# Performance work log

Hardware: AMD Instinct MI355X
Metric: run time of the kernel (lower is better)

The kernel has to match this reference:

```python
import jax, jax.numpy as jnp
import numpy as np

N = 100000   # total nodes in batch
E = 200000   # total edges
G = 4000     # number of graphs
H = 128      # gin_size = gin_hidden = gin_mlp_hidden = linear_hidden
L = 2        # gin_layers


def setup_inputs() -> dict:
    key = jax.random.key(0)
    ks = jax.random.split(key, 24)
    rn = lambda i, shape, s=0.05: (jax.random.normal(ks[i], shape, jnp.float32) * s)
    inp = dict(
        x=rn(0, (N, 14), 1.0),
        edge_attr=rn(1, (E, 4), 1.0),
        edge_index=jax.random.randint(ks[2], (2, E), 0, N, dtype=jnp.int32),
        batch=jnp.sort(jax.random.randint(ks[3], (N,), 0, G, dtype=jnp.int32)),
        node_w=rn(4, (14, H)), node_b=jnp.zeros((H,), jnp.float32),
        edge_w=rn(5, (4, H)), edge_b=jnp.zeros((H,), jnp.float32),
        eps=jnp.zeros((L,), jnp.float32),
        gin_w1=rn(6, (L, H, H)), gin_b1=jnp.zeros((L, H), jnp.float32),
        gin_w2=rn(7, (L, H, H)), gin_b2=jnp.zeros((L, H), jnp.float32),
        em_w1=rn(8, (L, H, H)), em_b1=jnp.zeros((L, H), jnp.float32),
        em_w2=rn(9, (L, H, H)), em_b2=jnp.zeros((L, H), jnp.float32),
        gru_wih=rn(10, (3 * H, H)), gru_whh=rn(11, (3 * H, H)),
        gru_bih=jnp.zeros((3 * H,), jnp.float32), gru_bhh=jnp.zeros((3 * H,), jnp.float32),
        lstm_wih=rn(12, (4 * H, 2 * H)), lstm_whh=rn(13, (4 * H, H)),
        lstm_bih=jnp.zeros((4 * H,), jnp.float32), lstm_bhh=jnp.zeros((4 * H,), jnp.float32),
        fc_w1=rn(14, (2 * H, H)), fc_b1=jnp.zeros((H,), jnp.float32),
        fc_w2=rn(15, (H, 1)), fc_b2=jnp.zeros((1,), jnp.float32),
    )
    return inp


def reference(x, edge_attr, edge_index, batch,
              node_w, node_b, edge_w, edge_b, eps,
              gin_w1, gin_b1, gin_w2, gin_b2,
              em_w1, em_b1, em_w2, em_b2,
              gru_wih, gru_whh, gru_bih, gru_bhh,
              lstm_wih, lstm_whh, lstm_bih, lstm_bhh,
              fc_w1, fc_b1, fc_w2, fc_b2):
    src, dst = edge_index[0], edge_index[1]
    node = x @ node_w + node_b          # [N,H]
    edge = edge_attr @ edge_w + edge_b  # [E,H]
    h = node                            # GRU hidden state
    for l in range(L):
        # GINEConv: msg = relu(x_src + e), scatter-add to dst, (1+eps)*x + agg, then MLP
        msg = jax.nn.relu(node[src] + edge)                     # [E,H] gather
        agg = jax.ops.segment_sum(msg, dst, num_segments=N)     # [N,H] scatter-add
        z = (1.0 + eps[l]) * node + agg
        m = jax.nn.relu(z @ gin_w1[l] + gin_b1[l]) @ gin_w2[l] + gin_b2[l]
        # GRU cell (seq_len=1)
        gi = m @ gru_wih.T + gru_bih
        gh = h @ gru_whh.T + gru_bhh
        ir, iz, inn = jnp.split(gi, 3, axis=-1)
        hr, hz, hn = jnp.split(gh, 3, axis=-1)
        r = jax.nn.sigmoid(ir + hr)
        zt = jax.nn.sigmoid(iz + hz)
        n = jnp.tanh(inn + r * hn)
        h = (1.0 - zt) * n + zt * h
        node = h
        # edge feature update MLP
        edge = jax.nn.relu(edge @ em_w1[l] + em_b1[l]) @ em_w2[l] + em_b2[l]
    # Set2Set pooling, processing_steps=3
    qs = jnp.zeros((G, 2 * H), node.dtype)
    hl = jnp.zeros((G, H), node.dtype)
    cl = jnp.zeros((G, H), node.dtype)
    for _ in range(3):
        g = qs @ lstm_wih.T + lstm_bih + hl @ lstm_whh.T + lstm_bhh
        i_, f_, g_, o_ = jnp.split(g, 4, axis=-1)
        cl = jax.nn.sigmoid(f_) * cl + jax.nn.sigmoid(i_) * jnp.tanh(g_)
        hl = jax.nn.sigmoid(o_) * jnp.tanh(cl)
        q = hl                                                   # [G,H]
        e = jnp.sum(node * q[batch], axis=-1)                    # [N]
        emax = jax.ops.segment_max(e, batch, num_segments=G)
        ex = jnp.exp(e - emax[batch])
        denom = jax.ops.segment_sum(ex, batch, num_segments=G)
        a = ex / jnp.maximum(denom, 1e-9)[batch]                 # per-graph softmax
        r = jax.ops.segment_sum(a[:, None] * node, batch, num_segments=G)  # [G,H]
        qs = jnp.concatenate([q, r], axis=-1)                    # [G,2H]
    out = jax.nn.relu(qs @ fc_w1 + fc_b1) @ fc_w2 + fc_b2
    return out.reshape(-1)
```

## Files before the change

kernel.cpp:

```cpp
#include <hip/hip_runtime.h>
#include <hip/hip_bf16.h>

constexpr int TN = 100000;
constexpr int TE = 200000;
constexpr int TG = 4000;
constexpr int TH = 128;

using short8 = __attribute__((ext_vector_type(8))) short;
using f32x4  = __attribute__((ext_vector_type(4))) float;
typedef __hip_bfloat16 bf16;

#define DEVINL __device__ __forceinline__
DEVINL float sigm(float x)  { return 1.f / (1.f + __expf(-x)); }
DEVINL float ftanh(float x) { return 1.f - 2.f / (__expf(2.f * x) + 1.f); }
DEVINL void unpack8(uint4 v, float* f) {
    const ushort* u = (const ushort*)&v;
#pragma unroll
    for (int j = 0; j < 8; ++j) f[j] = __bfloat162float(*(const bf16*)&u[j]);
}

__global__ void convAll(const float* __restrict__ g1, const float* __restrict__ g2,
                        const float* __restrict__ e1, const float* __restrict__ e2,
                        const float* __restrict__ gwih, const float* __restrict__ gwhh,
                        const float* __restrict__ lwih, const float* __restrict__ lwhh,
                        bf16* __restrict__ w6, bf16* __restrict__ wgru,
                        bf16* __restrict__ wl) {
    int i = blockIdx.x * 256 + threadIdx.x;
    if (i < 6 * TH * TH) {
        int m = i >> 14, r = i & 16383;
        int n = r >> 7, k = r & 127;
        const float* s = (m == 0) ? g1 : (m == 1) ? g1 + TH * TH
                       : (m == 2) ? g2 : (m == 3) ? g2 + TH * TH
                       : (m == 4) ? e1 : e2;
        w6[i] = __float2bfloat16(s[k * TH + n]);
        return;
    }
    i -= 6 * TH * TH;
    if (i < 2 * 384 * TH) {
        const float* s = (i < 384 * TH) ? gwih : gwhh;
        int r = (i < 384 * TH) ? i : i - 384 * TH;
        wgru[i] = __float2bfloat16(s[r]);
        return;
    }
    i -= 2 * 384 * TH;
    if (i < 512 * 256) {
        int c = i >> 8, k = i & 255;
        float v = (k < 128) ? lwih[c * 256 + k] + lwhh[c * 128 + k] : lwih[c * 256 + k];
        wl[i] = __float2bfloat16(v);
    }
}

template<int K>
__global__ __launch_bounds__(256) void proj64(const float* __restrict__ X,
                                              const float* __restrict__ W,
                                              const float* __restrict__ b,
                                              ushort* __restrict__ out, int M) {
    __shared__ float xs[64][K];
    int tid = threadIdx.x;
    int bm = blockIdx.x * 64;
    for (int i = tid; i < 64 * K; i += 256) {
        int r = i / K, k = i % K;
        xs[r][k] = (bm + r < M) ? X[(size_t)(bm + r) * K + k] : 0.f;
    }
    __syncthreads();
    int rb = tid >> 4, h0 = (tid & 15) * 8;
    float acc[4][8];
#pragma unroll
    for (int j = 0; j < 4; ++j)
#pragma unroll
        for (int c = 0; c < 8; ++c) acc[j][c] = b[h0 + c];
#pragma unroll
    for (int k = 0; k < K; ++k) {
        float4 w0 = *(const float4*)(W + k * TH + h0);
        float4 w1 = *(const float4*)(W + k * TH + h0 + 4);
#pragma unroll
        for (int j = 0; j < 4; ++j) {
            float xv = xs[rb + 16 * j][k];
            acc[j][0] = fmaf(xv, w0.x, acc[j][0]); acc[j][1] = fmaf(xv, w0.y, acc[j][1]);
            acc[j][2] = fmaf(xv, w0.z, acc[j][2]); acc[j][3] = fmaf(xv, w0.w, acc[j][3]);
            acc[j][4] = fmaf(xv, w1.x, acc[j][4]); acc[j][5] = fmaf(xv, w1.y, acc[j][5]);
            acc[j][6] = fmaf(xv, w1.z, acc[j][6]); acc[j][7] = fmaf(xv, w1.w, acc[j][7]);
        }
    }
#pragma unroll
    for (int j = 0; j < 4; ++j) {
        int row = bm + rb + 16 * j;
        if (row >= M) continue;
        ushort o[8];
#pragma unroll
        for (int c = 0; c < 8; ++c) {
            bf16 v = __float2bfloat16(acc[j][c]);
            o[c] = *(ushort*)&v;
        }
        *(uint4*)(out + (size_t)row * TH + h0) = *(uint4*)o;
    }
}

__global__ __launch_bounds__(256) void proj_scatter(
    const float* __restrict__ X, const float* __restrict__ W,
    const float* __restrict__ b, const int* __restrict__ perm,
    ushort* __restrict__ out, int M) {
    __shared__ float xs[64][4];
    int tid = threadIdx.x;
    int bm = blockIdx.x * 64;
    if (tid < 64) {
        float4 a = make_float4(0.f, 0.f, 0.f, 0.f);
        if (bm + tid < M) a = *(const float4*)(X + (size_t)(bm + tid) * 4);
        xs[tid][0] = a.x; xs[tid][1] = a.y; xs[tid][2] = a.z; xs[tid][3] = a.w;
    }
    __syncthreads();
    int rb = tid >> 4, h0 = (tid & 15) * 8;
    float acc[4][8];
#pragma unroll
    for (int j = 0; j < 4; ++j)
#pragma unroll
        for (int c = 0; c < 8; ++c) acc[j][c] = b[h0 + c];
#pragma unroll
    for (int k = 0; k < 4; ++k) {
        float4 w0 = *(const float4*)(W + k * TH + h0);
        float4 w1 = *(const float4*)(W + k * TH + h0 + 4);
#pragma unroll
        for (int j = 0; j < 4; ++j) {
            float xv = xs[rb + 16 * j][k];
            acc[j][0] = fmaf(xv, w0.x, acc[j][0]); acc[j][1] = fmaf(xv, w0.y, acc[j][1]);
            acc[j][2] = fmaf(xv, w0.z, acc[j][2]); acc[j][3] = fmaf(xv, w0.w, acc[j][3]);
            acc[j][4] = fmaf(xv, w1.x, acc[j][4]); acc[j][5] = fmaf(xv, w1.y, acc[j][5]);
            acc[j][6] = fmaf(xv, w1.z, acc[j][6]); acc[j][7] = fmaf(xv, w1.w, acc[j][7]);
        }
    }
#pragma unroll
    for (int j = 0; j < 4; ++j) {
        int row = bm + rb + 16 * j;
        if (row >= M) continue;
        ushort o[8];
#pragma unroll
        for (int c = 0; c < 8; ++c) {
            bf16 v = __float2bfloat16(acc[j][c]);
            o[c] = *(ushort*)&v;
        }
        *(uint4*)(out + (size_t)perm[row] * TH + h0) = *(uint4*)o;
    }
}

__global__ void count_deg(const int* __restrict__ ei_dst, int* __restrict__ deg, int En) {
    int e = blockIdx.x * 256 + threadIdx.x;
    if (e < En) atomicAdd(&deg[ei_dst[e]], 1);
}
__global__ void scan_block(const int* __restrict__ deg, int* __restrict__ rowptr,
                           int* __restrict__ bsum, int Nn) {
    __shared__ int sm[256];
    int tid = threadIdx.x;
    int gid = blockIdx.x * 256 + tid;
    int v = (gid < Nn) ? deg[gid] : 0;
    int x = v;
    sm[tid] = x; __syncthreads();
    for (int off = 1; off < 256; off <<= 1) {
        int t = (tid >= off) ? sm[tid - off] : 0;
        __syncthreads();
        x += t; sm[tid] = x;
        __syncthreads();
    }
    if (gid < Nn) rowptr[gid] = x - v;
    if (tid == 255) bsum[blockIdx.x] = x;
}
__global__ void scan_bsum(const int* __restrict__ bsum, int* __restrict__ bsumx, int nb) {
    __shared__ int sm[512];
    int tid = threadIdx.x;
    int v = (tid < nb) ? bsum[tid] : 0;
    int x = v;
    sm[tid] = x; __syncthreads();
    for (int off = 1; off < 512; off <<= 1) {
        int t = (tid >= off) ? sm[tid - off] : 0;
        __syncthreads();
        x += t; sm[tid] = x;
        __syncthreads();
    }
    if (tid < nb) bsumx[tid] = x - v;
}
__global__ void add_off(int* __restrict__ rowptr, const int* __restrict__ bsumx,
                        int Nn, int Etot) {
    int gid = blockIdx.x * 256 + threadIdx.x;
    if (gid < Nn) rowptr[gid] += bsumx[gid >> 8];
    if (gid == 0) rowptr[Nn] = Etot;
}
__global__ void fill_csr(const int* __restrict__ ei_src, const int* __restrict__ ei_dst,
                         const int* __restrict__ rowptr, int* __restrict__ cur,
                         int* __restrict__ srcp, int* __restrict__ epos, int En) {
    int e = blockIdx.x * 256 + threadIdx.x;
    if (e >= En) return;
    int d = ei_dst[e];
    int p = atomicAdd(&cur[d], 1);
    int slot = rowptr[d] + p;
    srcp[slot] = ei_src[e];
    epos[e] = slot;
}
__global__ void build_gptr(const int* __restrict__ batch, int* __restrict__ gptr,
                           int Nn, int Gn) {
    int n = blockIdx.x * 256 + threadIdx.x;
    if (n >= Nn) return;
    int bc = batch[n];
    int bp = (n == 0) ? -1 : batch[n - 1];
    for (int g = bp + 1; g <= bc; ++g) gptr[g] = n;
    if (n == Nn - 1) for (int g = bc + 1; g <= Gn; ++g) gptr[g] = Nn;
}

__global__ __launch_bounds__(256) void aggregate_v8(
    const ushort* __restrict__ node, const ushort* __restrict__ ef,
    const int* __restrict__ srcp, const int* __restrict__ rowptr,
    const float* __restrict__ eps, int l, ushort* __restrict__ zb, int Nn) {
    int t = blockIdx.x * 256 + threadIdx.x;
    int n = t >> 4;
    if (n >= Nn) return;
    int c8 = (t & 15) * 8;
    float se = 1.f + eps[l];
    float acc[8];
    uint4 nv = *(const uint4*)(node + (size_t)n * TH + c8);
    unpack8(nv, acc);
#pragma unroll
    for (int j = 0; j < 8; ++j) acc[j] *= se;
    int s0 = rowptr[n], s1 = rowptr[n + 1];
    int i = s0;
    for (; i + 1 < s1; i += 2) {
        int sa = srcp[i], sb = srcp[i + 1];
        uint4 av0 = *(const uint4*)(node + (size_t)sa * TH + c8);
        uint4 bv0 = *(const uint4*)(ef + (size_t)i * TH + c8);
        uint4 av1 = *(const uint4*)(node + (size_t)sb * TH + c8);
        uint4 bv1 = *(const uint4*)(ef + (size_t)(i + 1) * TH + c8);
        float a0[8], b0[8], a1[8], b1[8];
        unpack8(av0, a0); unpack8(bv0, b0);
        unpack8(av1, a1); unpack8(bv1, b1);
#pragma unroll
        for (int j = 0; j < 8; ++j)
            acc[j] += fmaxf(a0[j] + b0[j], 0.f) + fmaxf(a1[j] + b1[j], 0.f);
    }
    if (i < s1) {
        int sa = srcp[i];
        uint4 av = *(const uint4*)(node + (size_t)sa * TH + c8);
        uint4 bv = *(const uint4*)(ef + (size_t)i * TH + c8);
        float af[8], bf[8];
        unpack8(av, af); unpack8(bv, bf);
#pragma unroll
        for (int j = 0; j < 8; ++j) acc[j] += fmaxf(af[j] + bf[j], 0.f);
    }
    ushort o[8];
#pragma unroll
    for (int j = 0; j < 8; ++j) {
        bf16 v = __float2bfloat16(acc[j]);
        o[j] = *(ushort*)&v;
    }
    *(uint4*)(zb + (size_t)n * TH + c8) = *(uint4*)o;
}

__global__ __launch_bounds__(256) void mlp2_fused(
    const ushort* __restrict__ A, const ushort* __restrict__ W1t,
    const float* __restrict__ b1, const ushort* __restrict__ W2t,
    const float* __restrict__ b2, ushort* __restrict__ C, int M)
{
    __shared__ ushort As[128 * 128];
    __shared__ ushort Ts[128 * 128];
    const int tid = threadIdx.x;
    const int bm = blockIdx.x * 128;
    const int lane = tid & 63, w = tid >> 6;
    const int lr = lane & 15, lq = lane >> 4;
    const int wm = (w & 1) * 64, wn = (w >> 1) * 64;
    short8 wf[4][4];
#pragma unroll
    for (int ni = 0; ni < 4; ++ni)
#pragma unroll
        for (int ks = 0; ks < 4; ++ks)
            wf[ni][ks] = *(const short8*)(W1t + (size_t)(wn + ni * 16 + lr) * 128 + ks * 32 + lq * 8);
#pragma unroll
    for (int p = 0; p < 8; ++p) {
        int ch = p * 256 + tid;
        int r = ch >> 4, c = ch & 15;
        int row = bm + r;
        uint4 v = make_uint4(0u, 0u, 0u, 0u);
        if (row < M) v = *(const uint4*)(A + (size_t)row * 128 + c * 8);
        *(uint4*)(&As[r * 128 + ((c ^ (r & 15)) * 8)]) = v;
    }
    __syncthreads();
    {
        f32x4 acc[4][4] = {};
#pragma unroll
        for (int ks = 0; ks < 4; ++ks) {
            int cb = ks * 4 + lq;
            short8 af[4];
#pragma unroll
            for (int mi = 0; mi < 4; ++mi)
                af[mi] = *(const short8*)(&As[(wm + mi * 16 + lr) * 128 + ((cb ^ lr) * 8)]);
#pragma unroll
            for (int mi = 0; mi < 4; ++mi)
#pragma unroll
                for (int ni = 0; ni < 4; ++ni)
                    acc[mi][ni] = __builtin_amdgcn_mfma_f32_16x16x32_bf16(af[mi], wf[ni][ks], acc[mi][ni], 0, 0, 0);
        }
#pragma unroll
        for (int mi = 0; mi < 4; ++mi)
#pragma unroll
            for (int reg = 0; reg < 4; ++reg) {
                int row = wm + mi * 16 + lq * 4 + reg;
#pragma unroll
                for (int ni = 0; ni < 4; ++ni) {
                    int col = wn + ni * 16 + lr;
                    float v = fmaxf(acc[mi][ni][reg] + b1[col], 0.f);
                    bf16 bv = __float2bfloat16(v);
                    Ts[row * 128 + (((col >> 3) ^ (row & 15)) * 8) + (col & 7)] = *(ushort*)&bv;
                }
            }
    }
#pragma unroll
    for (int ni = 0; ni < 4; ++ni)
#pragma unroll
        for (int ks = 0; ks < 4; ++ks)
            wf[ni][ks] = *(const short8*)(W2t + (size_t)(wn + ni * 16 + lr) * 128 + ks * 32 + lq * 8);
    __syncthreads();
    {
        f32x4 acc[4][4] = {};
#pragma unroll
        for (int ks = 0; ks < 4; ++ks) {
            int cb = ks * 4 + lq;
            short8 af[4];
#pragma unroll
            for (int mi = 0; mi < 4; ++mi)
                af[mi] = *(const short8*)(&Ts[(wm + mi * 16 + lr) * 128 + ((cb ^ lr) * 8)]);
#pragma unroll
            for (int mi = 0; mi < 4; ++mi)
#pragma unroll
                for (int ni = 0; ni < 4; ++ni)
                    acc[mi][ni] = __builtin_amdgcn_mfma_f32_16x16x32_bf16(af[mi], wf[ni][ks], acc[mi][ni], 0, 0, 0);
        }
#pragma unroll
        for (int mi = 0; mi < 4; ++mi)
#pragma unroll
            for (int reg = 0; reg < 4; ++reg) {
                int row = bm + wm + mi * 16 + lq * 4 + reg;
                if (row >= M) continue;
#pragma unroll
                for (int ni = 0; ni < 4; ++ni) {
                    int col = wn + ni * 16 + lr;
                    bf16 bv = __float2bfloat16(acc[mi][ni][reg] + b2[col]);
                    C[(size_t)row * 128 + col] = *(ushort*)&bv;
                }
            }
    }
}

__global__ __launch_bounds__(512, 4) void gru_fused(
    const ushort* __restrict__ mfeat, const ushort* __restrict__ wih,
    const ushort* __restrict__ whh, const float* __restrict__ bih,
    const float* __restrict__ bhh, ushort* __restrict__ node, int Nn)
{
    __shared__ ushort Ms[64 * 128];
    __shared__ ushort Hs[64 * 128];
    const int tid = threadIdx.x;
    const int bm = blockIdx.x * 64;
#pragma unroll
    for (int p = 0; p < 4; ++p) {
        int ch = p * 512 + tid;
        bool isH = ch >= 1024;
        int r = (ch >> 4) & 63, c = ch & 15;
        int row = bm + r;
        uint4 v = make_uint4(0u, 0u, 0u, 0u);
        if (row < Nn) v = *(const uint4*)((isH ? node : mfeat) + (size_t)row * 128 + c * 8);
        ushort* dst = isH ? Hs : Ms;
        *(uint4*)(&dst[r * 128 + ((c ^ (r & 15)) * 8)]) = v;
    }
    __syncthreads();
    const int lane = tid & 63, w = tid >> 6;
    const int lr = lane & 15, lq = lane >> 4;
    const int col = w * 16 + lr;
    f32x4 aR[4] = {}, aZ[4] = {}, aN[4] = {}, aH[4] = {};
#pragma unroll
    for (int ks = 0; ks < 4; ++ks) {
        int koff = ks * 32 + lq * 8;
        short8 wv0 = *(const short8*)(wih + (size_t)col * 128 + koff);
        short8 wv1 = *(const short8*)(wih + (size_t)(128 + col) * 128 + koff);
        short8 wv2 = *(const short8*)(wih + (size_t)(256 + col) * 128 + koff);
        short8 wv3 = *(const short8*)(whh + (size_t)col * 128 + koff);
        short8 wv4 = *(const short8*)(whh + (size_t)(128 + col) * 128 + koff);
        short8 wv5 = *(const short8*)(whh + (size_t)(256 + col) * 128 + koff);
        int cb = ks * 4 + lq;
#pragma unroll
        for (int rt = 0; rt < 4; ++rt) {
            int off = (rt * 16 + lr) * 128 + ((cb ^ lr) * 8);
            short8 am = *(const short8*)(&Ms[off]);
            short8 ah = *(const short8*)(&Hs[off]);
            aR[rt] = __builtin_amdgcn_mfma_f32_16x16x32_bf16(am, wv0, aR[rt], 0, 0, 0);
            aR[rt] = __builtin_amdgcn_mfma_f32_16x16x32_bf16(ah, wv3, aR[rt], 0, 0, 0);
            aZ[rt] = __builtin_amdgcn_mfma_f32_16x16x32_bf16(am, wv1, aZ[rt], 0, 0, 0);
            aZ[rt] = __builtin_amdgcn_mfma_f32_16x16x32_bf16(ah, wv4, aZ[rt], 0, 0, 0);
            aN[rt] = __builtin_amdgcn_mfma_f32_16x16x32_bf16(am, wv2, aN[rt], 0, 0, 0);
            aH[rt] = __builtin_amdgcn_mfma_f32_16x16x32_bf16(ah, wv5, aH[rt], 0, 0, 0);
        }
    }
    {
        int h = col;
        float br = bih[h] + bhh[h];
        float bz = bih[128 + h] + bhh[128 + h];
        float bin = bih[256 + h], bhn = bhh[256 + h];
#pragma unroll
        for (int rt = 0; rt < 4; ++rt)
#pragma unroll
            for (int reg = 0; reg < 4; ++reg) {
                int lrow = rt * 16 + lq * 4 + reg;
                int row = bm + lrow;
                if (row >= Nn) continue;
                float r = sigm(aR[rt][reg] + br);
                float z = sigm(aZ[rt][reg] + bz);
                float n = ftanh(aN[rt][reg] + bin + r * (aH[rt][reg] + bhn));
                int hofs = lrow * 128 + (((h >> 3) ^ (lrow & 15)) * 8) + (h & 7);
                float hold = __bfloat162float(*(const bf16*)&Hs[hofs]);
                bf16 hv = __float2bfloat16((1.f - z) * n + z * hold);
                node[(size_t)row * 128 + h] = *(ushort*)&hv;
            }
    }
}

__global__ __launch_bounds__(256) void lstm_fused(
    ushort* __restrict__ s, const ushort* __restrict__ Wl,
    const float* __restrict__ bih, const float* __restrict__ bhh,
    float* __restrict__ cl, int Gn)
{
    __shared__ ushort Ss[16 * 256];
    const int tid = threadIdx.x;
    const int bm = blockIdx.x * 16;
#pragma unroll
    for (int p = 0; p < 2; ++p) {
        int ch = p * 256 + tid;
        int r = ch >> 5, c = ch & 31;
        int row = bm + r;
        uint4 v = make_uint4(0u, 0u, 0u, 0u);
        if (row < Gn) v = *(const uint4*)(s + (size_t)row * 256 + c * 8);
        *(uint4*)(&Ss[r * 256 + ((c ^ (r & 15)) * 8)]) = v;
    }
    __syncthreads();
    const int lane = tid & 63, w = tid >> 6;
    const int lr = lane & 15, lq = lane >> 4;
    f32x4 acc[4][2] = {};
#pragma unroll
    for (int ks = 0; ks < 8; ++ks) {
        int cb = ks * 4 + lq;
        short8 am = *(const short8*)(&Ss[lr * 256 + ((cb ^ lr) * 8)]);
        int koff = ks * 32 + lq * 8;
#pragma unroll
        for (int g = 0; g < 4; ++g)
#pragma unroll
            for (int sub = 0; sub < 2; ++sub) {
                int col = g * 128 + w * 32 + sub * 16 + lr;
                short8 bf = *(const short8*)(Wl + (size_t)col * 256 + koff);
                acc[g][sub] = __builtin_amdgcn_mfma_f32_16x16x32_bf16(am, bf, acc[g][sub], 0, 0, 0);
            }
    }
#pragma unroll
    for (int sub = 0; sub < 2; ++sub) {
        int h = w * 32 + sub * 16 + lr;
        float bi = bih[h] + bhh[h];
        float bff = bih[128 + h] + bhh[128 + h];
        float bg = bih[256 + h] + bhh[256 + h];
        float bo = bih[384 + h] + bhh[384 + h];
#pragma unroll
        for (int reg = 0; reg < 4; ++reg) {
            int row = bm + lq * 4 + reg;
            if (row >= Gn) continue;
            float iv = sigm(acc[0][sub][reg] + bi);
            float fv = sigm(acc[1][sub][reg] + bff);
            float gv = ftanh(acc[2][sub][reg] + bg);
            float ov = sigm(acc[3][sub][reg] + bo);
            float c = fv * cl[(size_t)row * 128 + h] + iv * gv;
            cl[(size_t)row * 128 + h] = c;
            bf16 hv = __float2bfloat16(ov * ftanh(c));
            s[(size_t)row * 256 + h] = *(ushort*)&hv;
        }
    }
}

__global__ __launch_bounds__(256) void att_fused(
    const ushort* __restrict__ node, ushort* __restrict__ s,
    const int* __restrict__ gptr)
{
    __shared__ float q[128];
    __shared__ float es[512];
    __shared__ float red[8];
    __shared__ float part[16][128];
    int g = blockIdx.x;
    int tid = threadIdx.x, lane = tid & 63, wid = tid >> 6;
    int n0 = gptr[g], n1 = gptr[g + 1];
    int cnt = n1 - n0; if (cnt > 512) cnt = 512;
    if (tid < 128) q[tid] = __bfloat162float(((const bf16*)s)[(size_t)g * 256 + tid]);
    __syncthreads();
    int gr = tid >> 4, c8 = (tid & 15) * 8;
    for (int i0 = 0; i0 < cnt; i0 += 16) {
        int i = i0 + gr;
        float p = 0.f;
        if (i < cnt) {
            uint4 v = *(const uint4*)(node + (size_t)(n0 + i) * TH + c8);
            float f[8]; unpack8(v, f);
#pragma unroll
            for (int j = 0; j < 8; ++j) p = fmaf(f[j], q[c8 + j], p);
        }
        p += __shfl_down(p, 8, 16);
        p += __shfl_down(p, 4, 16);
        p += __shfl_down(p, 2, 16);
        p += __shfl_down(p, 1, 16);
        if ((tid & 15) == 0 && i < cnt) es[i] = p;
    }
    __syncthreads();
    float m = -1e30f;
    for (int i = tid; i < cnt; i += 256) m = fmaxf(m, es[i]);
    for (int off = 32; off; off >>= 1) m = fmaxf(m, __shfl_down(m, off));
    if (lane == 0) red[wid] = m;
    __syncthreads();
    m = fmaxf(fmaxf(red[0], red[1]), fmaxf(red[2], red[3]));
    float sm = 0.f;
    for (int i = tid; i < cnt; i += 256) { float ex = __expf(es[i] - m); es[i] = ex; sm += ex; }
    for (int off = 32; off; off >>= 1) sm += __shfl_down(sm, off);
    if (lane == 0) red[4 + wid] = sm;
    __syncthreads();
    sm = red[4] + red[5] + red[6] + red[7];
    float inv = 1.f / fmaxf(sm, 1e-9f);
    float racc[8] = {};
    for (int i = gr; i < cnt; i += 16) {
        uint4 v = *(const uint4*)(node + (size_t)(n0 + i) * TH + c8);
        float f[8]; unpack8(v, f);
        float a = es[i];
#pragma unroll
        for (int j = 0; j < 8; ++j) racc[j] = fmaf(a, f[j], racc[j]);
    }
#pragma unroll
    for (int j = 0; j < 8; ++j) part[gr][c8 + j] = racc[j];
    __syncthreads();
    if (tid < 128) {
        float r = 0.f;
#pragma unroll
        for (int k = 0; k < 16; ++k) r += part[k][tid];
        bf16 rv = __float2bfloat16(r * inv);
        s[(size_t)g * 256 + 128 + tid] = *(ushort*)&rv;
    }
}

__global__ __launch_bounds__(128) void final_fc(const ushort* __restrict__ s,
                                                const float* __restrict__ w1,
                                                const float* __restrict__ b1,
                                                const float* __restrict__ w2,
                                                const float* __restrict__ b2,
                                                float* __restrict__ out) {
    __shared__ float q[256];
    __shared__ float red[2];
    int g = blockIdx.x, t = threadIdx.x;
    q[t] = __bfloat162float(((const bf16*)s)[(size_t)g * 256 + t]);
    q[t + 128] = __bfloat162float(((const bf16*)s)[(size_t)g * 256 + 128 + t]);
    __syncthreads();
    float acc = b1[t];
    for (int k = 0; k < 256; ++k) acc = fmaf(q[k], w1[k * TH + t], acc);
    acc = fmaxf(acc, 0.f);
    float p = acc * w2[t];
    for (int off = 32; off; off >>= 1) p += __shfl_down(p, off);
    if ((t & 63) == 0) red[t >> 6] = p;
    __syncthreads();
    if (t == 0) out[g] = red[0] + red[1] + b2[0];
}

static void launch_mlp2(const void* A, const bf16* W1t, const float* b1,
                        const bf16* W2t, const float* b2, void* C, int M, hipStream_t s) {
    hipLaunchKernelGGL(mlp2_fused, dim3((M + 127) / 128), dim3(256), 0, s,
                       (const ushort*)A, (const ushort*)W1t, b1, (const ushort*)W2t, b2,
                       (ushort*)C, M);
}

extern "C" void kernel_launch(void* const* d_in, const int* in_sizes, int n_in,
                              void* d_out, int out_size, void* d_ws, size_t ws_size,
                              hipStream_t stream) {
    const float* x         = (const float*)d_in[0];
    const float* edge_attr = (const float*)d_in[1];
    const int*   edge_index= (const int*)d_in[2];
    const int*   batch     = (const int*)d_in[3];
    const float* node_w    = (const float*)d_in[4];
    const float* node_b    = (const float*)d_in[5];
    const float* edge_w    = (const float*)d_in[6];
    const float* edge_b    = (const float*)d_in[7];
    const float* eps       = (const float*)d_in[8];
    const float* gin_w1    = (const float*)d_in[9];
    const float* gin_b1    = (const float*)d_in[10];
    const float* gin_w2    = (const float*)d_in[11];
    const float* gin_b2    = (const float*)d_in[12];
    const float* em_w1     = (const float*)d_in[13];
    const float* em_b1     = (const float*)d_in[14];
    const float* em_w2     = (const float*)d_in[15];
    const float* em_b2     = (const float*)d_in[16];
    const float* gru_wih   = (const float*)d_in[17];
    const float* gru_whh   = (const float*)d_in[18];
    const float* gru_bih   = (const float*)d_in[19];
    const float* gru_bhh   = (const float*)d_in[20];
    const float* lstm_wih  = (const float*)d_in[21];
    const float* lstm_whh  = (const float*)d_in[22];
    const float* lstm_bih  = (const float*)d_in[23];
    const float* lstm_bhh  = (const float*)d_in[24];
    const float* fc_w1     = (const float*)d_in[25];
    const float* fc_b1     = (const float*)d_in[26];
    const float* fc_w2     = (const float*)d_in[27];
    const float* fc_b2     = (const float*)d_in[28];
    float* out = (float*)d_out;
    const int* ei_src = edge_index;
    const int* ei_dst = edge_index + TE;

    char* base = (char*)d_ws;
    size_t off = 0;
    auto alloc = [&](size_t bytes) { void* p = base + off; off += (bytes + 15) & ~size_t(15); return p; };
    bf16*  nodeb = (bf16*)alloc((size_t)TN * TH * 2);
    bf16*  zb    = (bf16*)alloc((size_t)TN * TH * 2);
    bf16*  e1b   = (bf16*)alloc((size_t)TE * TH * 2);
    int*   deg   = (int*)alloc((size_t)TN * 4);
    int*   rowptr= (int*)alloc((size_t)(TN + 1) * 4);
    int*   cur   = (int*)alloc((size_t)TN * 4);
    int*   srcp  = (int*)alloc((size_t)TE * 4);
    int*   epos  = (int*)alloc((size_t)TE * 4);
    int*   bsum  = (int*)alloc(512 * 4);
    int*   bsumx = (int*)alloc(512 * 4);
    int*   gptr  = (int*)alloc((size_t)(TG + 1) * 4);
    bf16*  w6    = (bf16*)alloc(6 * TH * TH * 2);
    bf16*  wgru  = (bf16*)alloc(2 * 384 * TH * 2);
    bf16*  wl    = (bf16*)alloc(512 * 256 * 2);
    if (ws_size < off) return;

    bf16* w_gin1_0 = w6;
    bf16* w_gin1_1 = w6 + 1 * TH * TH;
    bf16* w_gin2_0 = w6 + 2 * TH * TH;
    bf16* w_gin2_1 = w6 + 3 * TH * TH;
    bf16* w_em1    = w6 + 4 * TH * TH;
    bf16* w_em2    = w6 + 5 * TH * TH;
    bf16* w_wih    = wgru;
    bf16* w_whh    = wgru + 384 * TH;

    ushort* sbuf = (ushort*)e1b;
    float*  cl   = (float*)(sbuf + (size_t)TG * 256);

    hipMemsetAsync(deg, 0, (size_t)TN * 4, stream);
    hipMemsetAsync(cur, 0, (size_t)TN * 4, stream);
    count_deg<<<(TE + 255) / 256, 256, 0, stream>>>(ei_dst, deg, TE);
    int nb = (TN + 255) / 256;
    scan_block<<<nb, 256, 0, stream>>>(deg, rowptr, bsum, TN);
    scan_bsum<<<1, 512, 0, stream>>>(bsum, bsumx, nb);
    add_off<<<nb, 256, 0, stream>>>(rowptr, bsumx, TN, TE);
    fill_csr<<<(TE + 255) / 256, 256, 0, stream>>>(ei_src, ei_dst, rowptr, cur, srcp, epos, TE);
    build_gptr<<<(TN + 255) / 256, 256, 0, stream>>>(batch, gptr, TN, TG);

    int convTot = 6 * TH * TH + 2 * 384 * TH + 512 * 256;
    convAll<<<(convTot + 255) / 256, 256, 0, stream>>>(
        gin_w1, gin_w2, em_w1, em_w2, gru_wih, gru_whh, lstm_wih, lstm_whh,
        w6, wgru, wl);

    proj64<14><<<(TN + 63) / 64, 256, 0, stream>>>(x, node_w, node_b, (ushort*)nodeb, TN);
    proj_scatter<<<(TE + 63) / 64, 256, 0, stream>>>(edge_attr, edge_w, edge_b,
                                                     epos, (ushort*)e1b, TE);

    aggregate_v8<<<(TN * 16 + 255) / 256, 256, 0, stream>>>(
        (const ushort*)nodeb, (const ushort*)e1b, srcp, rowptr, eps, 0, (ushort*)zb, TN);
    launch_mlp2(zb, w_gin1_0, gin_b1, w_gin2_0, gin_b2, zb, TN, stream);
    gru_fused<<<(TN + 63) / 64, 512, 0, stream>>>(
        (const ushort*)zb, (const ushort*)w_wih, (const ushort*)w_whh,
        gru_bih, gru_bhh, (ushort*)nodeb, TN);

    launch_mlp2(e1b, w_em1, em_b1, w_em2, em_b2, e1b, TE, stream);
    aggregate_v8<<<(TN * 16 + 255) / 256, 256, 0, stream>>>(
        (const ushort*)nodeb, (const ushort*)e1b, srcp, rowptr, eps, 1, (ushort*)zb, TN);
    launch_mlp2(zb, w_gin1_1, gin_b1 + TH, w_gin2_1, gin_b2 + TH, zb, TN, stream);
    gru_fused<<<(TN + 63) / 64, 512, 0, stream>>>(
        (const ushort*)zb, (const ushort*)w_wih, (const ushort*)w_whh,
        gru_bih, gru_bhh, (ushort*)nodeb, TN);

    hipMemsetAsync(sbuf, 0, (size_t)TG * 256 * 2 + (size_t)TG * 128 * 4, stream);
    for (int st = 0; st < 3; ++st) {
        lstm_fused<<<(TG + 15) / 16, 256, 0, stream>>>(
            sbuf, (const ushort*)wl, lstm_bih, lstm_bhh, cl, TG);
        att_fused<<<TG, 256, 0, stream>>>((const ushort*)nodeb, sbuf, gptr);
    }

    final_fc<<<TG, 128, 0, stream>>>(sbuf, fc_w1, fc_b1, fc_w2, fc_b2, out);
}
```

Before: 559.8 us.

## Fuse GIN MLP with GRU update into a single per-tile kernel

Replaces the separate two-layer GIN MLP launch and the GRU kernel with one kernel. Each 64-row tile of the aggregated features runs both MLP layers in shared memory, then the GRU gates, and writes the new node state back through shared memory as coalesced 16-byte stores. This removes the round trip of the MLP output through global memory and two launches per layer. In exchange, blocks shrink to 256 threads, each wave owns 16 rows and reloads all weight fragments from global/L2, and shared memory per block grows to 48KB, which may limit occupancy.

Result: slower. 802.0 us (+43.3%).

```diff
diff --git a/kernel.cpp b/kernel.cpp
--- a/kernel.cpp
+++ b/kernel.cpp
@@ -345,74 +345,138 @@
     }
 }
 
-__global__ __launch_bounds__(512, 4) void gru_fused(
-    const ushort* __restrict__ mfeat, const ushort* __restrict__ wih,
-    const ushort* __restrict__ whh, const float* __restrict__ bih,
-    const float* __restrict__ bhh, ushort* __restrict__ node, int Nn)
+__global__ __launch_bounds__(256, 3) void gin_gru_fused(
+    const ushort* __restrict__ Z, ushort* __restrict__ node,
+    const ushort* __restrict__ W1t, const float* __restrict__ b1,
+    const ushort* __restrict__ W2t, const float* __restrict__ b2,
+    const ushort* __restrict__ wih, const ushort* __restrict__ whh,
+    const float* __restrict__ bih, const float* __restrict__ bhh, int Nn)
 {
-    __shared__ ushort Ms[64 * 128];
+    __shared__ ushort Zs[64 * 128];
+    __shared__ ushort Ts[64 * 128];
     __shared__ ushort Hs[64 * 128];
     const int tid = threadIdx.x;
-    const int bm = blockIdx.x * 64;
-#pragma unroll
-    for (int p = 0; p < 4; ++p) {
-        int ch = p * 512 + tid;
+    const int bm  = blockIdx.x * 64;
+#pragma unroll
+    for (int p = 0; p < 8; ++p) {
+        int ch = p * 256 + tid;
         bool isH = ch >= 1024;
-        int r = (ch >> 4) & 63, c = ch & 15;
+        int rc = ch & 1023;
+        int r = rc >> 4, c = rc & 15;
         int row = bm + r;
         uint4 v = make_uint4(0u, 0u, 0u, 0u);
-        if (row < Nn) v = *(const uint4*)((isH ? node : mfeat) + (size_t)row * 128 + c * 8);
-        ushort* dst = isH ? Hs : Ms;
+        if (row < Nn) v = *(const uint4*)((isH ? node : Z) + (size_t)row * 128 + c * 8);
+        ushort* dst = isH ? Hs : Zs;
         *(uint4*)(&dst[r * 128 + ((c ^ (r & 15)) * 8)]) = v;
     }
     __syncthreads();
     const int lane = tid & 63, w = tid >> 6;
     const int lr = lane & 15, lq = lane >> 4;
-    const int col = w * 16 + lr;
-    f32x4 aR[4] = {}, aZ[4] = {}, aN[4] = {}, aH[4] = {};
+    const int wr = w * 16;
+    {
+        f32x4 acc[8] = {};
+#pragma unroll
+        for (int ks = 0; ks < 4; ++ks) {
+            int cb = ks * 4 + lq;
+            short8 af = *(const short8*)(&Zs[(wr + lr) * 128 + ((cb ^ lr) * 8)]);
+#pragma unroll
+            for (int ni = 0; ni < 8; ++ni) {
+                short8 wf = *(const short8*)(W1t + (size_t)(ni * 16 + lr) * 128 + ks * 32 + lq * 8);
+                acc[ni] = __builtin_amdgcn_mfma_f32_16x16x32_bf16(af, wf, acc[ni], 0, 0, 0);
+            }
+        }
+#pragma unroll
+        for (int ni = 0; ni < 8; ++ni) {
+            int col = ni * 16 + lr;
+            float bv = b1[col];
+            int cs = col >> 3, c7 = col & 7;
+#pragma unroll
+            for (int reg = 0; reg < 4; ++reg) {
+                int lrow = wr + lq * 4 + reg;
+                float v = fmaxf(acc[ni][reg] + bv, 0.f);
+                bf16 hv = __float2bfloat16(v);
+                Ts[lrow * 128 + ((cs ^ (lrow & 15)) * 8) + c7] = *(ushort*)&hv;
+            }
+        }
+    }
+    {
+        f32x4 acc[8] = {};
+#pragma unroll
+        for (int ks = 0; ks < 4; ++ks) {
+            int cb = ks * 4 + lq;
+            short8 af = *(const short8*)(&Ts[(wr + lr) * 128 + ((cb ^ lr) * 8)]);
+#pragma unroll
+            for (int ni = 0; ni < 8; ++ni) {
+                short8 wf = *(const short8*)(W2t + (size_t)(ni * 16 + lr) * 128 + ks * 32 + lq * 8);
+                acc[ni] = __builtin_amdgcn_mfma_f32_16x16x32_bf16(af, wf, acc[ni], 0, 0, 0);
+            }
+        }
+#pragma unroll
+        for (int ni = 0; ni < 8; ++ni) {
+            int col = ni * 16 + lr;
+            float bv = b2[col];
+            int cs = col >> 3, c7 = col & 7;
+#pragma unroll
+            for (int reg = 0; reg < 4; ++reg) {
+                int lrow = wr + lq * 4 + reg;
+                bf16 hv = __float2bfloat16(acc[ni][reg] + bv);
+                Zs[lrow * 128 + ((cs ^ (lrow & 15)) * 8) + c7] = *(ushort*)&hv;
+            }
+        }
+    }
+    short8 am[4], ah[4];
 #pragma unroll
     for (int ks = 0; ks < 4; ++ks) {
-        int koff = ks * 32 + lq * 8;
-        short8 wv0 = *(const short8*)(wih + (size_t)col * 128 + koff);
-        short8 wv1 = *(const short8*)(wih + (size_t)(128 + col) * 128 + koff);
-        short8 wv2 = *(const short8*)(wih + (size_t)(256 + col) * 128 + koff);
-        short8 wv3 = *(const short8*)(whh + (size_t)col * 128 + koff);
-        short8 wv4 = *(const short8*)(whh + (size_t)(128 + col) * 128 + koff);
-        short8 wv5 = *(const short8*)(whh + (size_t)(256 + col) * 128 + koff);
         int cb = ks * 4 + lq;
-#pragma unroll
-        for (int rt = 0; rt < 4; ++rt) {
-            int off = (rt * 16 + lr) * 128 + ((cb ^ lr) * 8);
-            short8 am = *(const short8*)(&Ms[off]);
-            short8 ah = *(const short8*)(&Hs[off]);
-            aR[rt] = __builtin_amdgcn_mfma_f32_16x16x32_bf16(am, wv0, aR[rt], 0, 0, 0);
-            aR[rt] = __builtin_amdgcn_mfma_f32_16x16x32_bf16(ah, wv3, aR[rt], 0, 0, 0);
-            aZ[rt] = __builtin_amdgcn_mfma_f32_16x16x32_bf16(am, wv1, aZ[rt], 0, 0, 0);
-            aZ[rt] = __builtin_amdgcn_mfma_f32_16x16x32_bf16(ah, wv4, aZ[rt], 0, 0, 0);
-            aN[rt] = __builtin_amdgcn_mfma_f32_16x16x32_bf16(am, wv2, aN[rt], 0, 0, 0);
-            aH[rt] = __builtin_amdgcn_mfma_f32_16x16x32_bf16(ah, wv5, aH[rt], 0, 0, 0);
-        }
-    }
-    {
-        int h = col;
-        float br = bih[h] + bhh[h];
-        float bz = bih[128 + h] + bhh[128 + h];
-        float bin = bih[256 + h], bhn = bhh[256 + h];
-#pragma unroll
-        for (int rt = 0; rt < 4; ++rt)
-#pragma unroll
-            for (int reg = 0; reg < 4; ++reg) {
-                int lrow = rt * 16 + lq * 4 + reg;
-                int row = bm + lrow;
-                if (row >= Nn) continue;
-                float r = sigm(aR[rt][reg] + br);
-                float z = sigm(aZ[rt][reg] + bz);
-                float n = ftanh(aN[rt][reg] + bin + r * (aH[rt][reg] + bhn));
-                int hofs = lrow * 128 + (((h >> 3) ^ (lrow & 15)) * 8) + (h & 7);
-                float hold = __bfloat162float(*(const bf16*)&Hs[hofs]);
-                bf16 hv = __float2bfloat16((1.f - z) * n + z * hold);
-                node[(size_t)row * 128 + h] = *(ushort*)&hv;
-            }
+        am[ks] = *(const short8*)(&Zs[(wr + lr) * 128 + ((cb ^ lr) * 8)]);
+        ah[ks] = *(const short8*)(&Hs[(wr + lr) * 128 + ((cb ^ lr) * 8)]);
+    }
+#pragma unroll
+    for (int cg = 0; cg < 8; ++cg) {
+        int col = cg * 16 + lr;
+        f32x4 aR = {}, aZ = {}, aN = {}, aH = {};
+#pragma unroll
+        for (int ks = 0; ks < 4; ++ks) {
+            int koff = ks * 32 + lq * 8;
+            short8 w0 = *(const short8*)(wih + (size_t)col * 128 + koff);
+            short8 w1 = *(const short8*)(wih + (size_t)(128 + col) * 128 + koff);
+            short8 w2 = *(const short8*)(wih + (size_t)(256 + col) * 128 + koff);
+            short8 w3 = *(const short8*)(whh + (size_t)col * 128 + koff);
+            short8 w4 = *(const short8*)(whh + (size_t)(128 + col) * 128 + koff);
+            short8 w5 = *(const short8*)(whh + (size_t)(256 + col) * 128 + koff);
+            aR = __builtin_amdgcn_mfma_f32_16x16x32_bf16(am[ks], w0, aR, 0, 0, 0);
+            aR = __builtin_amdgcn_mfma_f32_16x16x32_bf16(ah[ks], w3, aR, 0, 0, 0);
+            aZ = __builtin_amdgcn_mfma_f32_16x16x32_bf16(am[ks], w1, aZ, 0, 0, 0);
+            aZ = __builtin_amdgcn_mfma_f32_16x16x32_bf16(ah[ks], w4, aZ, 0, 0, 0);
+            aN = __builtin_amdgcn_mfma_f32_16x16x32_bf16(am[ks], w2, aN, 0, 0, 0);
+            aH = __builtin_amdgcn_mfma_f32_16x16x32_bf16(ah[ks], w5, aH, 0, 0, 0);
+        }
+        float br  = bih[col] + bhh[col];
+        float bz  = bih[128 + col] + bhh[128 + col];
+        float bin = bih[256 + col], bhn = bhh[256 + col];
+        int cs = col >> 3, c7 = col & 7;
+#pragma unroll
+        for (int reg = 0; reg < 4; ++reg) {
+            int lrow = wr + lq * 4 + reg;
+            int ofs = lrow * 128 + ((cs ^ (lrow & 15)) * 8) + c7;
+            float r = sigm(aR[reg] + br);
+            float z = sigm(aZ[reg] + bz);
+            float n = ftanh(aN[reg] + bin + r * (aH[reg] + bhn));
+            float hold = __bfloat162float(*(const bf16*)&Hs[ofs]);
+            bf16 hv = __float2bfloat16((1.f - z) * n + z * hold);
+            Ts[ofs] = *(ushort*)&hv;
+        }
+    }
+    __syncthreads();
+#pragma unroll
+    for (int p = 0; p < 4; ++p) {
+        int ch = p * 256 + tid;
+        int r = ch >> 4, c = ch & 15;
+        int row = bm + r;
+        if (row < Nn) {
+            uint4 v = *(const uint4*)(&Ts[r * 128 + ((c ^ (r & 15)) * 8)]);
+            *(uint4*)(node + (size_t)row * 128 + c * 8) = v;
+        }
     }
 }
 
@@ -655,18 +719,18 @@
 
     aggregate_v8<<<(TN * 16 + 255) / 256, 256, 0, stream>>>(
         (const ushort*)nodeb, (const ushort*)e1b, srcp, rowptr, eps, 0, (ushort*)zb, TN);
-    launch_mlp2(zb, w_gin1_0, gin_b1, w_gin2_0, gin_b2, zb, TN, stream);
-    gru_fused<<<(TN + 63) / 64, 512, 0, stream>>>(
-        (const ushort*)zb, (const ushort*)w_wih, (const ushort*)w_whh,
-        gru_bih, gru_bhh, (ushort*)nodeb, TN);
+    gin_gru_fused<<<(TN + 63) / 64, 256, 0, stream>>>(
+        (const ushort*)zb, (ushort*)nodeb,
+        (const ushort*)w_gin1_0, gin_b1, (const ushort*)w_gin2_0, gin_b2,
+        (const ushort*)w_wih, (const ushort*)w_whh, gru_bih, gru_bhh, TN);
 
     launch_mlp2(e1b, w_em1, em_b1, w_em2, em_b2, e1b, TE, stream);
     aggregate_v8<<<(TN * 16 + 255) / 256, 256, 0, stream>>>(
         (const ushort*)nodeb, (const ushort*)e1b, srcp, rowptr, eps, 1, (ushort*)zb, TN);
-    launch_mlp2(zb, w_gin1_1, gin_b1 + TH, w_gin2_1, gin_b2 + TH, zb, TN, stream);
-    gru_fused<<<(TN + 63) / 64, 512, 0, stream>>>(
-        (const ushort*)zb, (const ushort*)w_wih, (const ushort*)w_whh,
-        gru_bih, gru_bhh, (ushort*)nodeb, TN);
+    gin_gru_fused<<<(TN + 63) / 64, 256, 0, stream>>>(
+        (const ushort*)zb, (ushort*)nodeb,
+        (const ushort*)w_gin1_1, gin_b1 + TH, (const ushort*)w_gin2_1, gin_b2 + TH,
+        (const ushort*)w_wih, (const ushort*)w_whh, gru_bih, gru_bhh, TN);
 
     hipMemsetAsync(sbuf, 0, (size_t)TG * 256 * 2 + (size_t)TG * 128 * 4, stream);
     for (int st = 0; st < 3; ++st) {
```
